# Performance work log

Hardware: AMD Instinct MI355X
Metric: run time of the kernel (lower is better)

Reference implementation:

```python
import jax, jax.numpy as jnp
import numpy as np
import math

D_MODEL = 1024
NUM_HEADS = 16
HEAD_DIM = D_MODEL // NUM_HEADS
WINDOW = 5  # positions j with i - W//2 <= j <= i + W//2 are visible


def setup_inputs() -> dict:
    key = jax.random.key(0)
    ks = jax.random.split(key, 9)
    B, S = 2, 2048
    x = jax.random.normal(ks[0], (B, S, D_MODEL), dtype=jnp.float32)
    # Xavier-uniform linear weights [out, in] (torch convention), zero biases
    lim = math.sqrt(6.0 / (D_MODEL + D_MODEL))
    def w(k):
        return jax.random.uniform(k, (D_MODEL, D_MODEL), dtype=jnp.float32, minval=-lim, maxval=lim)
    return {
        'x': x,
        'Wq': w(ks[1]), 'bq': jnp.zeros((D_MODEL,), jnp.float32),
        'Wk': w(ks[2]), 'bk': jnp.zeros((D_MODEL,), jnp.float32),
        'Wv': w(ks[3]), 'bv': jnp.zeros((D_MODEL,), jnp.float32),
        'Wo': w(ks[4]), 'bo': jnp.zeros((D_MODEL,), jnp.float32),
    }


def reference(x, Wq, bq, Wk, bk, Wv, bv, Wo, bo):
    B, S, D = x.shape
    H, hd = NUM_HEADS, HEAD_DIM
    half = WINDOW // 2

    def proj(W, b):
        # torch Linear: y = x @ W.T + b ; split heads -> [B, H, S, hd]
        return (jnp.einsum('bsd,ed->bse', x, W) + b).reshape(B, S, H, hd).transpose(0, 2, 1, 3)

    q = proj(Wq, bq)
    k = proj(Wk, bk)
    v = proj(Wv, bv)

    scores = jnp.einsum('bhqd,bhkd->bhqk', q, k) / jnp.sqrt(jnp.asarray(hd, x.dtype))
    i = jnp.arange(S)[:, None]
    j = jnp.arange(S)[None, :]
    band = (j >= i - half) & (j <= i + half)  # [S, S] local window mask
    scores = jnp.where(band, scores, jnp.asarray(-1e9, x.dtype))
    attn = jax.nn.softmax(scores, axis=-1)  # dropout is identity in eval mode
    out = jnp.einsum('bhqk,bhkd->bhqd', attn, v)
    out = out.transpose(0, 2, 1, 3).reshape(B, S, D)
    return jnp.einsum('bsd,ed->bse', out, Wo) + bo
```

## Files before the change

### kernel.cpp

```cpp
#include <hip/hip_runtime.h>
#include <hip/hip_bf16.h>

typedef __bf16 bf16_t;
typedef __bf16 bf16x4 __attribute__((ext_vector_type(4)));
typedef __bf16 bf16x8 __attribute__((ext_vector_type(8)));
typedef float f32x4 __attribute__((ext_vector_type(4)));

#define S_LEN 2048
#define DMODEL 1024
#define NHEADS 16
#define HDIM 64
#define BROWS 4096

__device__ __forceinline__ void async16(const void* g, void* l) {
  __builtin_amdgcn_global_load_lds(
      (const __attribute__((address_space(1))) void*)g,
      (__attribute__((address_space(3))) void*)l, 16, 0, 0);
}

__global__ __launch_bounds__(256) void cvt_all_kernel(
    const float* __restrict__ x, const float* __restrict__ Wq,
    const float* __restrict__ Wk, const float* __restrict__ Wv,
    const float* __restrict__ Wo, bf16_t* __restrict__ dst) {
  const int i = blockIdx.x * 256 + threadIdx.x;
  constexpr int XN4 = (BROWS * DMODEL) / 4;
  constexpr int WN4 = (DMODEL * DMODEL) / 4;
  const float* src;
  size_t off;
  if (i < XN4) {
    src = x;
    off = (size_t)i;
  } else {
    const int wi = i - XN4;
    const int w = wi >> 18;
    off = (size_t)(wi & (WN4 - 1));
    src = (w == 0) ? Wq : (w == 1) ? Wk : (w == 2) ? Wv : Wo;
  }
  const float4 v = *(const float4*)(src + off * 4);
  bf16x4 o;
  o[0] = (bf16_t)v.x;
  o[1] = (bf16_t)v.y;
  o[2] = (bf16_t)v.z;
  o[3] = (bf16_t)v.w;
  *(bf16x4*)(dst + (size_t)i * 4) = o;
}

#define BARR __builtin_amdgcn_s_barrier()
#define LGKM0 asm volatile("s_waitcnt lgkmcnt(0)" ::: "memory")
#define VMC4 asm volatile("s_waitcnt vmcnt(4)" ::: "memory")
#define VMC0 asm volatile("s_waitcnt vmcnt(0)" ::: "memory")

template <typename OutT>
__device__ __forceinline__ void gemm256_body(
    const bf16_t* __restrict__ A, const bf16_t* __restrict__ W,
    const float* __restrict__ bias, OutT* __restrict__ C, int m0, int n0,
    char* lds) {
  constexpr int Kd = 1024, Nd = 1024;
  char* ldsA = lds;
  char* ldsB = lds + 65536;

  const int tid = threadIdx.x;
  const int lane = tid & 63;
  const int wid = tid >> 6;
  const int wr = wid >> 2;
  const int wc = wid & 3;
  const int fr = lane & 15;
  const int l16 = lane >> 4;

  f32x4 acc[8][4] = {};
  bf16x8 aA[4][2], bB[4][2];

  auto stage = [&](const bf16_t* G, char* ldsX, int gr0, int buf, int h,
                   int kt) {
#pragma unroll
    for (int l = 0; l < 2; ++l) {
      const int idx = l * 512 + tid;
      const int r = idx >> 3;
      const int slot = idx & 7;
      async16((const char*)(G + (size_t)(gr0 + h * 128 + r) * Kd + kt * 64 +
                            ((slot ^ (r & 7)) << 3)),
              ldsX + buf * 32768 + h * 16384 + r * 128 + slot * 16);
    }
  };

  auto rdA = [&](int buf, int row, int ks) -> bf16x8 {
    return *(const bf16x8*)(ldsA + buf * 32768 + row * 128 +
                            ((((ks << 2) + l16) ^ (row & 7)) << 4));
  };
  auto rdB = [&](int buf, int row, int ks) -> bf16x8 {
    return *(const bf16x8*)(ldsB + buf * 32768 + row * 128 +
                            ((((ks << 2) + l16) ^ (row & 7)) << 4));
  };

#define RDA(MH, BUF)                                          \
  _Pragma("unroll") for (int m_ = 0; m_ < 4; ++m_)            \
      _Pragma("unroll") for (int ks_ = 0; ks_ < 2; ++ks_)     \
          aA[m_][ks_] = rdA(BUF, wr * 128 + (MH)*64 + m_ * 16 + fr, ks_);
#define RDB(NH, BUF)                                          \
  _Pragma("unroll") for (int n_ = 0; n_ < 2; ++n_)            \
      _Pragma("unroll") for (int ks_ = 0; ks_ < 2; ++ks_)     \
          bB[(NH)*2 + n_][ks_] = rdB(BUF, wc * 64 + (NH)*32 + n_ * 16 + fr, ks_);
#define MMAQ(MH, NH)                                                          \
  _Pragma("unroll") for (int m_ = 0; m_ < 4; ++m_)                            \
      _Pragma("unroll") for (int n_ = 0; n_ < 2; ++n_) {                      \
    acc[(MH)*4 + m_][(NH)*2 + n_] = __builtin_amdgcn_mfma_f32_16x16x32_bf16(  \
        aA[m_][0], bB[(NH)*2 + n_][0], acc[(MH)*4 + m_][(NH)*2 + n_], 0, 0,   \
        0);                                                                   \
    acc[(MH)*4 + m_][(NH)*2 + n_] = __builtin_amdgcn_mfma_f32_16x16x32_bf16(  \
        aA[m_][1], bB[(NH)*2 + n_][1], acc[(MH)*4 + m_][(NH)*2 + n_], 0, 0,   \
        0);                                                                   \
  }

  stage(A, ldsA, m0, 0, 0, 0);
  stage(A, ldsA, m0, 0, 1, 0);
  stage(W, ldsB, n0, 0, 0, 0);
  stage(W, ldsB, n0, 0, 1, 0);
  stage(W, ldsB, n0, 1, 0, 1);
  stage(W, ldsB, n0, 1, 1, 1);
  VMC4;
  BARR;

#pragma unroll 1
  for (int i = 0; i < 8; ++i) {
    const int t0 = 2 * i, t1 = 2 * i + 1;
    const bool st = (i < 7);
    RDA(0, 0);
    RDB(0, 0);
    stage(A, ldsA, m0, 1, 0, t1);
    BARR;
    LGKM0;
    __builtin_amdgcn_s_setprio(1);
    MMAQ(0, 0);
    __builtin_amdgcn_s_setprio(0);
    BARR;
    RDB(1, 0);
    stage(A, ldsA, m0, 1, 1, t1);
    BARR;
    LGKM0;
    __builtin_amdgcn_s_setprio(1);
    MMAQ(0, 1);
    __builtin_amdgcn_s_setprio(0);
    BARR;
    RDA(1, 0);
    if (st) stage(W, ldsB, n0, 0, 0, t0 + 2);
    BARR;
    LGKM0;
    __builtin_amdgcn_s_setprio(1);
    MMAQ(1, 0);
    __builtin_amdgcn_s_setprio(0);
    BARR;
    if (st) stage(W, ldsB, n0, 0, 1, t0 + 2);
    __builtin_amdgcn_s_setprio(1);
    MMAQ(1, 1);
    __builtin_amdgcn_s_setprio(0);
    if (st) {
      VMC4;
    } else {
      VMC0;
    }
    BARR;
    RDA(0, 1);
    RDB(0, 1);
    if (st) stage(A, ldsA, m0, 0, 0, t0 + 2);
    BARR;
    LGKM0;
    __builtin_amdgcn_s_setprio(1);
    MMAQ(0, 0);
    __builtin_amdgcn_s_setprio(0);
    BARR;
    RDB(1, 1);
    if (st) stage(A, ldsA, m0, 0, 1, t0 + 2);
    BARR;
    LGKM0;
    __builtin_amdgcn_s_setprio(1);
    MMAQ(0, 1);
    __builtin_amdgcn_s_setprio(0);
    BARR;
    RDA(1, 1);
    if (st) stage(W, ldsB, n0, 1, 0, t1 + 2);
    BARR;
    LGKM0;
    __builtin_amdgcn_s_setprio(1);
    MMAQ(1, 0);
    __builtin_amdgcn_s_setprio(0);
    BARR;
    if (st) stage(W, ldsB, n0, 1, 1, t1 + 2);
    __builtin_amdgcn_s_setprio(1);
    MMAQ(1, 1);
    __builtin_amdgcn_s_setprio(0);
    if (st) VMC4;
    BARR;
  }
#undef RDA
#undef RDB
#undef MMAQ

  const int cr = l16 * 4;
#pragma unroll
  for (int nf = 0; nf < 4; ++nf) {
    const int col = n0 + wc * 64 + nf * 16 + fr;
    const float bv = bias[col];
#pragma unroll
    for (int mf = 0; mf < 8; ++mf) {
      const int row = m0 + wr * 128 + mf * 16 + cr;
#pragma unroll
      for (int r = 0; r < 4; ++r)
        C[(size_t)(row + r) * Nd + col] = (OutT)(acc[mf][nf][r] + bv);
    }
  }
}

__global__ __launch_bounds__(512, 2) void gemm_qkv256_kernel(
    const bf16_t* __restrict__ xb, const bf16_t* __restrict__ Wqkv,
    const float* __restrict__ bq, const float* __restrict__ bk,
    const float* __restrict__ bv, bf16_t* __restrict__ Q,
    bf16_t* __restrict__ K, bf16_t* __restrict__ V) {
  __shared__ char lds[131072];
  const int nt = blockIdx.y;
  const int mat = nt >> 2;
  const int n0 = (nt & 3) * 256;
  const bf16_t* W = Wqkv + (size_t)mat * DMODEL * DMODEL;
  const float* bias = (mat == 0) ? bq : (mat == 1) ? bk : bv;
  bf16_t* C = (mat == 0) ? Q : (mat == 1) ? K : V;
  gemm256_body<bf16_t>(xb, W, bias, C, blockIdx.x * 256, n0, lds);
}

template <typename OutT>
__device__ __forceinline__ void gemm_body(
    const bf16_t* __restrict__ A, const bf16_t* __restrict__ W,
    const float* __restrict__ bias, OutT* __restrict__ C, int m0, int n0) {
  constexpr int Kd = 1024, Nd = 1024, BK = 32, NT = Kd / BK;
  __shared__ bf16_t ldsA[2][128 * BK];
  __shared__ bf16_t ldsB[2][128 * BK];

  const int tid = threadIdx.x;
  const int lane = tid & 63;
  const int wave = tid >> 6;
  const int wr = wave >> 1;
  const int wc = wave & 1;

  f32x4 acc[4][4] = {};

  const int fr = lane & 15;
  const int ko = (lane >> 4) * 8;

  auto stage = [&](int buf, int t) {
    const int k0 = t * BK;
#pragma unroll
    for (int p = 0; p < 2; ++p) {
      const int off = (p * 256 + tid) * 16;
      const int row = off >> 6;
      const int kb = off & 63;
      async16((const char*)(A + (size_t)(m0 + row) * Kd + k0) + kb,
              (char*)ldsA[buf] + off);
      async16((const char*)(W + (size_t)(n0 + row) * Kd + k0) + kb,
              (char*)ldsB[buf] + off);
    }
  };

  auto compute = [&](int buf) {
    bf16x8 af[4], bfr[4];
#pragma unroll
    for (int i = 0; i < 4; ++i)
      af[i] = *(const bf16x8*)(ldsA[buf] + (wr * 64 + i * 16 + fr) * BK + ko);
#pragma unroll
    for (int j = 0; j < 4; ++j)
      bfr[j] = *(const bf16x8*)(ldsB[buf] + (wc * 64 + j * 16 + fr) * BK + ko);
#pragma unroll
    for (int i = 0; i < 4; ++i)
#pragma unroll
      for (int j = 0; j < 4; ++j)
        acc[i][j] = __builtin_amdgcn_mfma_f32_16x16x32_bf16(af[i], bfr[j],
                                                            acc[i][j], 0, 0, 0);
  };

  stage(0, 0);
  __syncthreads();
#pragma unroll 1
  for (int t = 0; t < NT; ++t) {
    if (t + 1 < NT) stage((t + 1) & 1, t + 1);
    compute(t & 1);
    __syncthreads();
  }

  const int cr = (lane >> 4) * 4;
#pragma unroll
  for (int j = 0; j < 4; ++j) {
    const int col = n0 + wc * 64 + j * 16 + fr;
    const float bv = bias[col];
#pragma unroll
    for (int i = 0; i < 4; ++i) {
#pragma unroll
      for (int r = 0; r < 4; ++r) {
        const int row = m0 + wr * 64 + i * 16 + cr + r;
        C[(size_t)row * Nd + col] = (OutT)(acc[i][j][r] + bv);
      }
    }
  }
}

__global__ __launch_bounds__(256) void gemm_o_kernel(
    const bf16_t* __restrict__ ctx, const bf16_t* __restrict__ Wob,
    const float* __restrict__ bo, float* __restrict__ out) {
  gemm_body<float>(ctx, Wob, bo, out, blockIdx.x * 128, blockIdx.y * 128);
}

#define CHUNK 256
#define TROWS 260

__global__ __launch_bounds__(256) void attn_kernel(
    const bf16_t* __restrict__ Q, const bf16_t* __restrict__ K,
    const bf16_t* __restrict__ V, bf16_t* __restrict__ ctx) {
  __shared__ bf16_t ldsK[TROWS * HDIM];
  __shared__ bf16_t ldsV[TROWS * HDIM];

  const int tid = threadIdx.x;
  const int blk = blockIdx.x;
  const int chunk = blk & 7;
  const int bh = blk >> 3;
  const int h = bh & (NHEADS - 1);
  const int b = bh >> 4;
  const int s0 = chunk * CHUNK;

  const bf16_t* Kb = K + (size_t)b * S_LEN * DMODEL + h * HDIM;
  const bf16_t* Vb = V + (size_t)b * S_LEN * DMODEL + h * HDIM;

#pragma unroll
  for (int j = 0; j < 9; ++j) {
    const int i = j * 256 + tid;
    if (i < TROWS * 8) {
      const int tr = i >> 3;
      const int slot = i & 7;
      const int c = slot ^ (tr & 7);
      int gs = s0 - 2 + tr;
      gs = (gs < 0) ? 0 : (gs >= S_LEN ? S_LEN - 1 : gs);
      async16((const char*)(Kb + (size_t)gs * DMODEL) + c * 16,
              (char*)ldsK + i * 16);
      async16((const char*)(Vb + (size_t)gs * DMODEL) + c * 16,
              (char*)ldsV + i * 16);
    }
  }

  const int s = s0 + tid;
  const bf16_t* Qrow = Q + ((size_t)(b * S_LEN) + s) * DMODEL + h * HDIM;
  bf16x8 q8[8];
#pragma unroll
  for (int c = 0; c < 8; ++c) q8[c] = *(const bf16x8*)(Qrow + c * 8);
  float qf[64];
#pragma unroll
  for (int c = 0; c < 8; ++c)
#pragma unroll
    for (int e = 0; e < 8; ++e) qf[c * 8 + e] = (float)q8[c][e];

  __syncthreads();

  float sc[5];
#pragma unroll
  for (int jj = 0; jj < 5; ++jj) {
    const int tr = tid + jj;
    float d = 0.f;
#pragma unroll
    for (int c = 0; c < 8; ++c) {
      const bf16x8 k8 = *(const bf16x8*)(ldsK + tr * HDIM + (c ^ (tr & 7)) * 8);
#pragma unroll
      for (int e = 0; e < 8; ++e) d += qf[c * 8 + e] * (float)k8[e];
    }
    const int j = s - 2 + jj;
    sc[jj] = (j < 0 || j >= S_LEN) ? -1e30f : d * 0.125f;
  }

  float m = sc[0];
#pragma unroll
  for (int jj = 1; jj < 5; ++jj) m = fmaxf(m, sc[jj]);
  float p[5], l = 0.f;
#pragma unroll
  for (int jj = 0; jj < 5; ++jj) {
    p[jj] = __expf(sc[jj] - m);
    l += p[jj];
  }
  const float inv = 1.0f / l;
#pragma unroll
  for (int jj = 0; jj < 5; ++jj) p[jj] *= inv;

  float o[64];
#pragma unroll
  for (int e = 0; e < 64; ++e) o[e] = 0.f;
#pragma unroll
  for (int jj = 0; jj < 5; ++jj) {
    const int tr = tid + jj;
    const float pj = p[jj];
#pragma unroll
    for (int c = 0; c < 8; ++c) {
      const bf16x8 v8 = *(const bf16x8*)(ldsV + tr * HDIM + (c ^ (tr & 7)) * 8);
#pragma unroll
      for (int e = 0; e < 8; ++e) o[c * 8 + e] += pj * (float)v8[e];
    }
  }

  bf16_t* Crow = (bf16_t*)ctx + ((size_t)(b * S_LEN) + s) * DMODEL + h * HDIM;
#pragma unroll
  for (int c = 0; c < 8; ++c) {
    bf16x8 ov;
#pragma unroll
    for (int e = 0; e < 8; ++e) ov[e] = (bf16_t)o[c * 8 + e];
    *(bf16x8*)(Crow + c * 8) = ov;
  }
}

extern "C" void kernel_launch(void* const* d_in, const int* in_sizes, int n_in,
                              void* d_out, int out_size, void* d_ws,
                              size_t ws_size, hipStream_t stream) {
  const float* x = (const float*)d_in[0];
  const float* Wq = (const float*)d_in[1];
  const float* bq = (const float*)d_in[2];
  const float* Wk = (const float*)d_in[3];
  const float* bk = (const float*)d_in[4];
  const float* Wv = (const float*)d_in[5];
  const float* bv = (const float*)d_in[6];
  const float* Wo = (const float*)d_in[7];
  const float* bo = (const float*)d_in[8];
  float* out = (float*)d_out;

  const size_t mat = (size_t)BROWS * DMODEL;
  const size_t wmat = (size_t)DMODEL * DMODEL;
  bf16_t* xb = (bf16_t*)d_ws;
  bf16_t* Wqb = xb + mat;
  bf16_t* Wob = Wqb + 3 * wmat;
  bf16_t* Q = Wob + wmat;
  bf16_t* K = Q + mat;
  bf16_t* V = K + mat;
  bf16_t* ctx = V + mat;

  cvt_all_kernel<<<8192, 256, 0, stream>>>(x, Wq, Wk, Wv, Wo, xb);

  gemm_qkv256_kernel<<<dim3(16, 12), 512, 0, stream>>>(xb, Wqb, bq, bk, bv, Q,
                                                       K, V);
  attn_kernel<<<256, 256, 0, stream>>>(Q, K, V, ctx);
  gemm_o_kernel<<<dim3(32, 8), 256, 0, stream>>>(ctx, Wob, bo, out);
}
```

Before: 80.67 us.

## Retile fused QKV GEMM to 256x192 tiles over a single interleaved QKV output

The QKV projection now treats the three weight matrices as one 3072-wide N dimension and uses 256x192 tiles. This gives a 16x16 grid (256 blocks) instead of 16x12 (192), so the work spreads more evenly across the CUs. Output goes to a single [4096,3072] interleaved buffer, and the attention kernel reads Q/K/V with stride 3072. The trade-offs are smaller B tiles per wave (3 fragments instead of 4), which lowers MMA reuse, and strided attention loads.

Result: no change. 80.07 us (-0.7%).

```diff
diff --git a/kernel.cpp b/kernel.cpp
--- a/kernel.cpp
+++ b/kernel.cpp
@@ -11,6 +11,7 @@
 #define NHEADS 16
 #define HDIM 64
 #define BROWS 4096
+#define QKVN 3072
 
 __device__ __forceinline__ void async16(const void* g, void* l) {
   __builtin_amdgcn_global_load_lds(
@@ -47,17 +48,20 @@
 
 #define BARR __builtin_amdgcn_s_barrier()
 #define LGKM0 asm volatile("s_waitcnt lgkmcnt(0)" ::: "memory")
-#define VMC4 asm volatile("s_waitcnt vmcnt(4)" ::: "memory")
+#define VMC3 asm volatile("s_waitcnt vmcnt(3)" ::: "memory")
 #define VMC0 asm volatile("s_waitcnt vmcnt(0)" ::: "memory")
 
-template <typename OutT>
-__device__ __forceinline__ void gemm256_body(
+__global__ __launch_bounds__(512, 2) void gemm_qkv256_kernel(
     const bf16_t* __restrict__ A, const bf16_t* __restrict__ W,
-    const float* __restrict__ bias, OutT* __restrict__ C, int m0, int n0,
-    char* lds) {
-  constexpr int Kd = 1024, Nd = 1024;
+    const float* __restrict__ bq, const float* __restrict__ bk,
+    const float* __restrict__ bv, bf16_t* __restrict__ C) {
+  constexpr int Kd = 1024;
+  __shared__ char lds[114688];
   char* ldsA = lds;
   char* ldsB = lds + 65536;
+
+  const int m0 = blockIdx.x * 256;
+  const int n0 = blockIdx.y * 192;
 
   const int tid = threadIdx.x;
   const int lane = tid & 63;
@@ -67,20 +71,26 @@
   const int fr = lane & 15;
   const int l16 = lane >> 4;
 
-  f32x4 acc[8][4] = {};
-  bf16x8 aA[4][2], bB[4][2];
-
-  auto stage = [&](const bf16_t* G, char* ldsX, int gr0, int buf, int h,
-                   int kt) {
+  f32x4 acc[8][3] = {};
+  bf16x8 aA[4][2], bB[3][2];
+
+  auto stageA = [&](int buf, int h, int kt) {
 #pragma unroll
     for (int l = 0; l < 2; ++l) {
       const int idx = l * 512 + tid;
       const int r = idx >> 3;
       const int slot = idx & 7;
-      async16((const char*)(G + (size_t)(gr0 + h * 128 + r) * Kd + kt * 64 +
+      async16((const char*)(A + (size_t)(m0 + h * 128 + r) * Kd + kt * 64 +
                             ((slot ^ (r & 7)) << 3)),
-              ldsX + buf * 32768 + h * 16384 + r * 128 + slot * 16);
-    }
+              ldsA + buf * 32768 + h * 16384 + r * 128 + slot * 16);
+    }
+  };
+  auto stageB = [&](int buf, int th, int kt) {
+    const int r = tid >> 3;
+    const int slot = tid & 7;
+    async16((const char*)(W + (size_t)(n0 + th * 64 + r) * Kd + kt * 64 +
+                          ((slot ^ (r & 7)) << 3)),
+            ldsB + buf * 24576 + th * 8192 + r * 128 + slot * 16);
   };
 
   auto rdA = [&](int buf, int row, int ks) -> bf16x8 {
@@ -88,36 +98,37 @@
                             ((((ks << 2) + l16) ^ (row & 7)) << 4));
   };
   auto rdB = [&](int buf, int row, int ks) -> bf16x8 {
-    return *(const bf16x8*)(ldsB + buf * 32768 + row * 128 +
+    return *(const bf16x8*)(ldsB + buf * 24576 + row * 128 +
                             ((((ks << 2) + l16) ^ (row & 7)) << 4));
   };
 
-#define RDA(MH, BUF)                                          \
-  _Pragma("unroll") for (int m_ = 0; m_ < 4; ++m_)            \
-      _Pragma("unroll") for (int ks_ = 0; ks_ < 2; ++ks_)     \
-          aA[m_][ks_] = rdA(BUF, wr * 128 + (MH)*64 + m_ * 16 + fr, ks_);
-#define RDB(NH, BUF)                                          \
-  _Pragma("unroll") for (int n_ = 0; n_ < 2; ++n_)            \
-      _Pragma("unroll") for (int ks_ = 0; ks_ < 2; ++ks_)     \
-          bB[(NH)*2 + n_][ks_] = rdB(BUF, wc * 64 + (NH)*32 + n_ * 16 + fr, ks_);
-#define MMAQ(MH, NH)                                                          \
+#define RDA(MH, BUF)                                                     \
+  _Pragma("unroll") for (int m_ = 0; m_ < 4; ++m_)                       \
+      _Pragma("unroll") for (int ks_ = 0; ks_ < 2; ++ks_) aA[m_][ks_] =  \
+          rdA(BUF, wr * 128 + (MH)*64 + m_ * 16 + fr, ks_);
+#define RDB(NF0, NC, BUF)                                                \
+  _Pragma("unroll") for (int n_ = 0; n_ < (NC); ++n_)                    \
+      _Pragma("unroll") for (int ks_ = 0; ks_ < 2; ++ks_)                \
+          bB[(NF0) + n_][ks_] =                                          \
+              rdB(BUF, wc * 48 + ((NF0) + n_) * 16 + fr, ks_);
+#define MMAQ(MH, NF0, NC)                                                     \
   _Pragma("unroll") for (int m_ = 0; m_ < 4; ++m_)                            \
-      _Pragma("unroll") for (int n_ = 0; n_ < 2; ++n_) {                      \
-    acc[(MH)*4 + m_][(NH)*2 + n_] = __builtin_amdgcn_mfma_f32_16x16x32_bf16(  \
-        aA[m_][0], bB[(NH)*2 + n_][0], acc[(MH)*4 + m_][(NH)*2 + n_], 0, 0,   \
-        0);                                                                   \
-    acc[(MH)*4 + m_][(NH)*2 + n_] = __builtin_amdgcn_mfma_f32_16x16x32_bf16(  \
-        aA[m_][1], bB[(NH)*2 + n_][1], acc[(MH)*4 + m_][(NH)*2 + n_], 0, 0,   \
-        0);                                                                   \
-  }
-
-  stage(A, ldsA, m0, 0, 0, 0);
-  stage(A, ldsA, m0, 0, 1, 0);
-  stage(W, ldsB, n0, 0, 0, 0);
-  stage(W, ldsB, n0, 0, 1, 0);
-  stage(W, ldsB, n0, 1, 0, 1);
-  stage(W, ldsB, n0, 1, 1, 1);
-  VMC4;
+      _Pragma("unroll") for (int n_ = 0; n_ < (NC); ++n_) {                   \
+    acc[(MH)*4 + m_][(NF0) + n_] = __builtin_amdgcn_mfma_f32_16x16x32_bf16(   \
+        aA[m_][0], bB[(NF0) + n_][0], acc[(MH)*4 + m_][(NF0) + n_], 0, 0, 0); \
+    acc[(MH)*4 + m_][(NF0) + n_] = __builtin_amdgcn_mfma_f32_16x16x32_bf16(   \
+        aA[m_][1], bB[(NF0) + n_][1], acc[(MH)*4 + m_][(NF0) + n_], 0, 0, 0); \
+  }
+
+  stageA(0, 0, 0);
+  stageA(0, 1, 0);
+  stageB(0, 0, 0);
+  stageB(0, 1, 0);
+  stageB(0, 2, 0);
+  stageB(1, 0, 1);
+  stageB(1, 1, 1);
+  stageB(1, 2, 1);
+  VMC3;
   BARR;
 
 #pragma unroll 1
@@ -125,70 +136,76 @@
     const int t0 = 2 * i, t1 = 2 * i + 1;
     const bool st = (i < 7);
     RDA(0, 0);
-    RDB(0, 0);
-    stage(A, ldsA, m0, 1, 0, t1);
-    BARR;
-    LGKM0;
-    __builtin_amdgcn_s_setprio(1);
-    MMAQ(0, 0);
-    __builtin_amdgcn_s_setprio(0);
-    BARR;
-    RDB(1, 0);
-    stage(A, ldsA, m0, 1, 1, t1);
-    BARR;
-    LGKM0;
-    __builtin_amdgcn_s_setprio(1);
-    MMAQ(0, 1);
+    RDB(0, 2, 0);
+    stageA(1, 0, t1);
+    BARR;
+    LGKM0;
+    __builtin_amdgcn_s_setprio(1);
+    MMAQ(0, 0, 2);
+    __builtin_amdgcn_s_setprio(0);
+    BARR;
+    RDB(2, 1, 0);
+    stageA(1, 1, t1);
+    BARR;
+    LGKM0;
+    __builtin_amdgcn_s_setprio(1);
+    MMAQ(0, 2, 1);
     __builtin_amdgcn_s_setprio(0);
     BARR;
     RDA(1, 0);
-    if (st) stage(W, ldsB, n0, 0, 0, t0 + 2);
-    BARR;
-    LGKM0;
-    __builtin_amdgcn_s_setprio(1);
-    MMAQ(1, 0);
-    __builtin_amdgcn_s_setprio(0);
-    BARR;
-    if (st) stage(W, ldsB, n0, 0, 1, t0 + 2);
-    __builtin_amdgcn_s_setprio(1);
-    MMAQ(1, 1);
-    __builtin_amdgcn_s_setprio(0);
+    if (st) stageB(0, 0, t0 + 2);
+    BARR;
+    LGKM0;
+    __builtin_amdgcn_s_setprio(1);
+    MMAQ(1, 0, 2);
+    __builtin_amdgcn_s_setprio(0);
+    BARR;
     if (st) {
-      VMC4;
+      stageB(0, 1, t0 + 2);
+      stageB(0, 2, t0 + 2);
+    }
+    __builtin_amdgcn_s_setprio(1);
+    MMAQ(1, 2, 1);
+    __builtin_amdgcn_s_setprio(0);
+    if (st) {
+      VMC3;
     } else {
       VMC0;
     }
     BARR;
     RDA(0, 1);
-    RDB(0, 1);
-    if (st) stage(A, ldsA, m0, 0, 0, t0 + 2);
-    BARR;
-    LGKM0;
-    __builtin_amdgcn_s_setprio(1);
-    MMAQ(0, 0);
-    __builtin_amdgcn_s_setprio(0);
-    BARR;
-    RDB(1, 1);
-    if (st) stage(A, ldsA, m0, 0, 1, t0 + 2);
-    BARR;
-    LGKM0;
-    __builtin_amdgcn_s_setprio(1);
-    MMAQ(0, 1);
+    RDB(0, 2, 1);
+    if (st) stageA(0, 0, t0 + 2);
+    BARR;
+    LGKM0;
+    __builtin_amdgcn_s_setprio(1);
+    MMAQ(0, 0, 2);
+    __builtin_amdgcn_s_setprio(0);
+    BARR;
+    RDB(2, 1, 1);
+    if (st) stageA(0, 1, t0 + 2);
+    BARR;
+    LGKM0;
+    __builtin_amdgcn_s_setprio(1);
+    MMAQ(0, 2, 1);
     __builtin_amdgcn_s_setprio(0);
     BARR;
     RDA(1, 1);
-    if (st) stage(W, ldsB, n0, 1, 0, t1 + 2);
-    BARR;
-    LGKM0;
-    __builtin_amdgcn_s_setprio(1);
-    MMAQ(1, 0);
-    __builtin_amdgcn_s_setprio(0);
-    BARR;
-    if (st) stage(W, ldsB, n0, 1, 1, t1 + 2);
-    __builtin_amdgcn_s_setprio(1);
-    MMAQ(1, 1);
-    __builtin_amdgcn_s_setprio(0);
-    if (st) VMC4;
+    if (st) stageB(1, 0, t1 + 2);
+    BARR;
+    LGKM0;
+    __builtin_amdgcn_s_setprio(1);
+    MMAQ(1, 0, 2);
+    __builtin_amdgcn_s_setprio(0);
+    BARR;
+    if (st) {
+      stageB(1, 1, t1 + 2);
+      stageB(1, 2, t1 + 2);
+    }
+    __builtin_amdgcn_s_setprio(1);
+    MMAQ(1, 2, 1);
+    __builtin_amdgcn_s_setprio(0);
+    if (st) VMC3;
     BARR;
   }
 #undef RDA
@@ -197,32 +214,19 @@
 
   const int cr = l16 * 4;
 #pragma unroll
-  for (int nf = 0; nf < 4; ++nf) {
-    const int col = n0 + wc * 64 + nf * 16 + fr;
-    const float bv = bias[col];
+  for (int nf = 0; nf < 3; ++nf) {
+    const int col = n0 + wc * 48 + nf * 16 + fr;
+    const int mat = col >> 10;
+    const float* bp = (mat == 0) ? bq : (mat == 1) ? bk : bv;
+    const float bval = bp[col & 1023];
 #pragma unroll
     for (int mf = 0; mf < 8; ++mf) {
       const int row = m0 + wr * 128 + mf * 16 + cr;
 #pragma unroll
       for (int r = 0; r < 4; ++r)
-        C[(size_t)(row + r) * Nd + col] = (OutT)(acc[mf][nf][r] + bv);
-    }
-  }
-}
-
-__global__ __launch_bounds__(512, 2) void gemm_qkv256_kernel(
-    const bf16_t* __restrict__ xb, const bf16_t* __restrict__ Wqkv,
-    const float* __restrict__ bq, const float* __restrict__ bk,
-    const float* __restrict__ bv, bf16_t* __restrict__ Q,
-    bf16_t* __restrict__ K, bf16_t* __restrict__ V) {
-  __shared__ char lds[131072];
-  const int nt = blockIdx.y;
-  const int mat = nt >> 2;
-  const int n0 = (nt & 3) * 256;
-  const bf16_t* W = Wqkv + (size_t)mat * DMODEL * DMODEL;
-  const float* bias = (mat == 0) ? bq : (mat == 1) ? bk : bv;
-  bf16_t* C = (mat == 0) ? Q : (mat == 1) ? K : V;
-  gemm256_body<bf16_t>(xb, W, bias, C, blockIdx.x * 256, n0, lds);
+        C[(size_t)(row + r) * QKVN + col] = (bf16_t)(acc[mf][nf][r] + bval);
+    }
+  }
 }
 
 template <typename OutT>
@@ -287,13 +291,13 @@
 #pragma unroll
   for (int j = 0; j < 4; ++j) {
     const int col = n0 + wc * 64 + j * 16 + fr;
-    const float bv = bias[col];
+    const float bval = bias[col];
 #pragma unroll
     for (int i = 0; i < 4; ++i) {
 #pragma unroll
       for (int r = 0; r < 4; ++r) {
         const int row = m0 + wr * 64 + i * 16 + cr + r;
-        C[(size_t)row * Nd + col] = (OutT)(acc[i][j][r] + bv);
+        C[(size_t)row * Nd + col] = (OutT)(acc[i][j][r] + bval);
       }
     }
   }
@@ -309,8 +313,7 @@
 #define TROWS 260
 
 __global__ __launch_bounds__(256) void attn_kernel(
-    const bf16_t* __restrict__ Q, const bf16_t* __restrict__ K,
-    const bf16_t* __restrict__ V, bf16_t* __restrict__ ctx) {
+    const bf16_t* __restrict__ QKV, bf16_t* __restrict__ ctx) {
   __shared__ bf16_t ldsK[TROWS * HDIM];
   __shared__ bf16_t ldsV[TROWS * HDIM];
 
@@ -322,8 +325,8 @@
   const int b = bh >> 4;
   const int s0 = chunk * CHUNK;
 
-  const bf16_t* Kb = K + (size_t)b * S_LEN * DMODEL + h * HDIM;
-  const bf16_t* Vb = V + (size_t)b * S_LEN * DMODEL + h * HDIM;
+  const bf16_t* Kb = QKV + (size_t)b * S_LEN * QKVN + DMODEL + h * HDIM;
+  const bf16_t* Vb = QKV + (size_t)b * S_LEN * QKVN + 2 * DMODEL + h * HDIM;
 
 #pragma unroll
   for (int j = 0; j < 9; ++j) {
@@ -334,15 +337,15 @@
       const int c = slot ^ (tr & 7);
       int gs = s0 - 2 + tr;
       gs = (gs < 0) ? 0 : (gs >= S_LEN ? S_LEN - 1 : gs);
-      async16((const char*)(Kb + (size_t)gs * DMODEL) + c * 16,
+      async16((const char*)(Kb + (size_t)gs * QKVN) + c * 16,
               (char*)ldsK + i * 16);
-      async16((const char*)(Vb + (size_t)gs * DMODEL) + c * 16,
+      async16((const char*)(Vb + (size_t)gs * QKVN) + c * 16,
               (char*)ldsV + i * 16);
     }
   }
 
   const int s = s0 + tid;
-  const bf16_t* Qrow = Q + ((size_t)(b * S_LEN) + s) * DMODEL + h * HDIM;
+  const bf16_t* Qrow = QKV + ((size_t)(b * S_LEN) + s) * QKVN + h * HDIM;
   bf16x8 q8[8];
 #pragma unroll
   for (int c = 0; c < 8; ++c) q8[c] = *(const bf16x8*)(Qrow + c * 8);
@@ -424,17 +427,15 @@
   const size_t mat = (size_t)BROWS * DMODEL;
   const size_t wmat = (size_t)DMODEL * DMODEL;
   bf16_t* xb = (bf16_t*)d_ws;
-  bf16_t* Wqb = xb + mat;
-  bf16_t* Wob = Wqb + 3 * wmat;
-  bf16_t* Q = Wob + wmat;
-  bf16_t* K = Q + mat;
-  bf16_t* V = K + mat;
-  bf16_t* ctx = V + mat;
+  bf16_t* Wqkv = xb + mat;
+  bf16_t* Wob = Wqkv + 3 * wmat;
+  bf16_t* QKV = Wob + wmat;
+  bf16_t* ctx = QKV + 3 * mat;
 
   cvt_all_kernel<<<8192, 256, 0, stream>>>(x, Wq, Wk, Wv, Wo, xb);
 
-  gemm_qkv256_kernel<<<dim3(16, 12), 512, 0, stream>>>(xb, Wqb, bq, bk, bv, Q,
-                                                       K, V);
-  attn_kernel<<<256, 256, 0, stream>>>(Q, K, V, ctx);
+  gemm_qkv256_kernel<<<dim3(16, 16), 512, 0, stream>>>(xb, Wqkv, bq, bk, bv,
+                                                       QKV);
+  attn_kernel<<<256, 256, 0, stream>>>(QKV, ctx);
   gemm_o_kernel<<<dim3(32, 8), 256, 0, stream>>>(ctx, Wob, bo, out);
 }
```
